# Optimization experiments

Measured on AMD Instinct MI355X. Metric: run time of the kernel, lower is better.

Reference implementation:

```python
import jax, jax.numpy as jnp
import numpy as np

N_NODES = 50000
N_EDGES = 1600000
IN_DIM = 1024
HID = 128
N_GRAPHS = 64


def setup_inputs() -> dict:
    key = jax.random.key(0)
    ks = jax.random.split(key, 8)
    x = jax.random.normal(ks[0], (N_NODES, IN_DIM), dtype=jnp.float32)
    edge_index = jax.random.randint(ks[1], (2, N_EDGES), 0, N_NODES, dtype=jnp.int32)
    batch = jnp.sort(jax.random.randint(ks[2], (N_NODES,), 0, N_GRAPHS, dtype=jnp.int32))
    # GATConv parameters (single head, concat irrelevant for 1 head)
    glorot = 1.0 / np.sqrt(IN_DIM)
    W = jax.random.uniform(ks[3], (IN_DIM, HID), minval=-glorot, maxval=glorot, dtype=jnp.float32)
    ga = 1.0 / np.sqrt(HID)
    att_src = jax.random.uniform(ks[4], (HID,), minval=-ga, maxval=ga, dtype=jnp.float32)
    att_dst = jax.random.uniform(ks[5], (HID,), minval=-ga, maxval=ga, dtype=jnp.float32)
    bias = jnp.zeros((HID,), dtype=jnp.float32)
    return {"x": x, "W": W, "att_src": att_src, "att_dst": att_dst, "bias": bias,
            "edge_index": edge_index, "batch": batch, "num_graphs": N_GRAPHS}


def reference(x, W, att_src, att_dst, bias, edge_index, batch, num_graphs):
    N = x.shape[0]
    h = x @ W                               # [N, HID]
    # add self-loops (GATConv default add_self_loops=True)
    loops = jnp.arange(N, dtype=edge_index.dtype)
    src = jnp.concatenate([edge_index[0], loops])   # [E+N]
    dst = jnp.concatenate([edge_index[1], loops])
    a_src = h @ att_src                     # [N]
    a_dst = h @ att_dst                     # [N]
    e = jax.nn.leaky_relu(a_src[src] + a_dst[dst], negative_slope=0.2)  # [E+N]
    # scatter-softmax over incoming edges of each destination node
    m = jax.ops.segment_max(e, dst, num_segments=N)
    p = jnp.exp(e - m[dst])
    denom = jax.ops.segment_sum(p, dst, num_segments=N)
    alpha = p / denom[dst]                  # [E+N]
    # attention-weighted aggregation
    out = jax.ops.segment_sum(alpha[:, None] * h[src], dst, num_segments=N)  # [N, HID]
    out = jax.nn.relu(out + bias)
    # global max pool over graphs in the batch
    return jax.ops.segment_max(out, batch, num_segments=num_graphs)          # [G, HID]
```

## Files before the change

### kernel.cpp

```cpp
#include <hip/hip_runtime.h>
#include <hip/hip_bf16.h>

#define N_NODES 50000
#define N_EDGES 1600000
#define IN_DIM 1024
#define HID 128
#define AGG_WAVES 6144

typedef __bf16 bf16x8 __attribute__((ext_vector_type(8)));
typedef float f32x4 __attribute__((ext_vector_type(4)));
typedef __bf16 bf16x4 __attribute__((ext_vector_type(4)));

__device__ __forceinline__ float2 bf2f(unsigned u) {
    return make_float2(__uint_as_float(u << 16), __uint_as_float(u & 0xffff0000u));
}
__device__ __forceinline__ float lrelu(float v) { return v > 0.f ? v : 0.2f * v; }
__device__ __forceinline__ float f16tof(unsigned bits) {
    return (float)__builtin_bit_cast(_Float16, (unsigned short)bits);
}

__global__ void prep_kernel(const float* __restrict__ W, __bf16* __restrict__ wt,
                            int* __restrict__ deg, float* __restrict__ out, int out_n) {
    int i = blockIdx.x * 256 + threadIdx.x;
    if (i < N_NODES) deg[i] = 0;
    if (i < out_n) out[i] = 0.0f;
    if (i < HID * IN_DIM) {
        int n = i >> 10, k = i & 1023;
        wt[i] = (__bf16)W[(size_t)k * HID + n];
    }
}

__global__ __launch_bounds__(256) void gemm_kernel(const float* __restrict__ x,
                                                   const __bf16* __restrict__ wt,
                                                   __bf16* __restrict__ h2,
                                                   const float* __restrict__ att_s,
                                                   const float* __restrict__ att_d,
                                                   float* __restrict__ o_as,
                                                   float* __restrict__ o_ad,
                                                   float* __restrict__ o_ps) {
    __shared__ __bf16 xa[2][64][40];
    __shared__ __bf16 wb[2][128][40];
    const int t = threadIdx.x;
    const int m0 = blockIdx.x * 64;
    const int wid = t >> 6, lane = t & 63;
    const int lm = lane & 15, q8 = (lane >> 4) * 8;
    const int rw0 = wid * 16;

    float4 xs_reg[2];
    uint2  ws_reg[4];

    auto stage_regs = [&](int k0) {
#pragma unroll
        for (int l = 0; l < 2; ++l) {
            int f = t + l * 256;
            int row = f >> 3, kq = f & 7;
            int gr = m0 + row;
            float4 v = make_float4(0.f, 0.f, 0.f, 0.f);
            if (gr < N_NODES)
                v = *(const float4*)(x + (size_t)gr * IN_DIM + k0 + kq * 4);
            xs_reg[l] = v;
        }
#pragma unroll
        for (int l = 0; l < 4; ++l) {
            int f = t + l * 256;
            int n = f >> 3, c = f & 7;
            ws_reg[l] = *(const uint2*)(wt + (size_t)n * IN_DIM + k0 + c * 4);
        }
    };
    auto regs_to_lds = [&](int b) {
#pragma unroll
        for (int l = 0; l < 2; ++l) {
            int f = t + l * 256;
            int row = f >> 3, kq = f & 7;
            bf16x4 v;
            v[0] = (__bf16)xs_reg[l].x; v[1] = (__bf16)xs_reg[l].y;
            v[2] = (__bf16)xs_reg[l].z; v[3] = (__bf16)xs_reg[l].w;
            *(bf16x4*)&xa[b][row][kq * 4] = v;
        }
#pragma unroll
        for (int l = 0; l < 4; ++l) {
            int f = t + l * 256;
            int n = f >> 3, c = f & 7;
            *(uint2*)&wb[b][n][c * 4] = ws_reg[l];
        }
    };

    f32x4 acc[8] = {};
    stage_regs(0);
    regs_to_lds(0);
    __syncthreads();
    for (int it = 0; it < 32; ++it) {
        const int cur = it & 1;
        if (it + 1 < 32) stage_regs((it + 1) * 32);
        bf16x8 af = *(const bf16x8*)&xa[cur][rw0 + lm][q8];
#pragma unroll
        for (int ct = 0; ct < 8; ++ct) {
            bf16x8 bfr = *(const bf16x8*)&wb[cur][ct * 16 + lm][q8];
            acc[ct] = __builtin_amdgcn_mfma_f32_16x16x32_bf16(af, bfr, acc[ct], 0, 0, 0);
        }
        if (it + 1 < 32) {
            regs_to_lds(cur ^ 1);
            __syncthreads();
        }
    }
    const int quad = lane >> 4;
    float attsf[8], attdf[8];
#pragma unroll
    for (int ct = 0; ct < 8; ++ct) {
        attsf[ct] = att_s[ct * 16 + lm];
        attdf[ct] = att_d[ct * 16 + lm];
    }
#pragma unroll
    for (int reg = 0; reg < 4; ++reg) {
        int row = m0 + rw0 + quad * 4 + reg;
        float ps = 0.f, pd = 0.f;
#pragma unroll
        for (int ct = 0; ct < 8; ++ct) {
            float v = acc[ct][reg];
            ps = fmaf(v, attsf[ct], ps);
            pd = fmaf(v, attdf[ct], pd);
        }
#pragma unroll
        for (int o = 8; o; o >>= 1) {
            ps += __shfl_xor(ps, o);
            pd += __shfl_xor(pd, o);
        }
        if (row < N_NODES) {
            if (lm == 0) {
                o_as[row] = ps; o_ad[row] = pd;
                o_ps[row] = __expf(lrelu(ps + pd));
            }
#pragma unroll
            for (int ct = 0; ct < 8; ++ct)
                h2[(size_t)row * HID + ct * 16 + lm] = (__bf16)acc[ct][reg];
        }
    }
}

__global__ void hist_kernel(const int* __restrict__ ei, int* __restrict__ deg) {
    int e = blockIdx.x * 256 + threadIdx.x;
    if (e < N_EDGES) atomicAdd(&deg[ei[N_EDGES + e]], 1);
}

__global__ void scan1_kernel(const int* __restrict__ deg, int* __restrict__ bsum) {
    int b = blockIdx.x, t = threadIdx.x;
    int base = b * 1024 + t * 4;
    int s = 0;
#pragma unroll
    for (int j = 0; j < 4; ++j) {
        int idx = base + j;
        if (idx < N_NODES) s += deg[idx];
    }
    for (int o = 32; o; o >>= 1) s += __shfl_xor(s, o);
    __shared__ int wsum[4];
    int lane = t & 63, w = t >> 6;
    if (lane == 0) wsum[w] = s;
    __syncthreads();
    if (t == 0) bsum[b] = wsum[0] + wsum[1] + wsum[2] + wsum[3];
}

__global__ void scan2_kernel(const int* __restrict__ bsum, int* __restrict__ boff,
                             int* __restrict__ rowstart, int nb) {
    if (threadIdx.x == 0 && blockIdx.x == 0) {
        int run = 0;
        for (int i = 0; i < nb; ++i) { boff[i] = run; run += bsum[i]; }
        rowstart[N_NODES] = run;
    }
}

__global__ void scan3_kernel(const int* __restrict__ deg, const int* __restrict__ boff,
                             int* __restrict__ rowstart, int* __restrict__ cursor) {
    int b = blockIdx.x, t = threadIdx.x;
    int base = b * 1024 + t * 4;
    int v[4]; int s = 0;
#pragma unroll
    for (int j = 0; j < 4; ++j) {
        int idx = base + j;
        v[j] = (idx < N_NODES) ? deg[idx] : 0;
        s += v[j];
    }
    int lane = t & 63, w = t >> 6;
    int inc = s;
    for (int o = 1; o < 64; o <<= 1) {
        int u = __shfl_up(inc, o);
        if (lane >= o) inc += u;
    }
    __shared__ int wt[4];
    if (lane == 63) wt[w] = inc;
    __syncthreads();
    int woff = 0;
    for (int i = 0; i < w; ++i) woff += wt[i];
    int run = woff + inc - s + boff[b];
#pragma unroll
    for (int j = 0; j < 4; ++j) {
        int idx = base + j;
        if (idx < N_NODES) {
            rowstart[idx] = run;
            cursor[idx] = run;
            run += v[j];
        }
    }
}

__global__ void scatter_kernel(const int* __restrict__ ei, int* __restrict__ cursor,
                               unsigned* __restrict__ csrp, const float* __restrict__ a_src,
                               const float* __restrict__ a_dst) {
    int e = blockIdx.x * 256 + threadIdx.x;
    if (e >= N_EDGES) return;
    int s = ei[e], d = ei[N_EDGES + e];
    int slot = atomicAdd(&cursor[d], 1);
    float pe = __expf(lrelu(a_src[s] + a_dst[d]));
    unsigned short hb = __builtin_bit_cast(unsigned short, (_Float16)pe);
    csrp[slot] = (unsigned)s | ((unsigned)hb << 16);
}

__global__ __launch_bounds__(256, 6) void aggregate_kernel(
    const unsigned* __restrict__ h2u, const float* __restrict__ pself_a,
    const int* __restrict__ rowstart, const unsigned* __restrict__ csrp,
    const float* __restrict__ bias, const int* __restrict__ batch,
    float* __restrict__ out) {
    const int wid = threadIdx.x >> 6, lane = threadIdx.x & 63;
    const int w = blockIdx.x * 4 + wid;
    const int q = N_NODES / AGG_WAVES;
    const int r = N_NODES - q * AGG_WAVES;
    int n0 = w * q + (w < r ? w : r);
    int n1 = n0 + q + (w < r ? 1 : 0);
    const float b0 = bias[2 * lane], b1 = bias[2 * lane + 1];

    int gcur = -1;
    float m0 = 0.f, m1 = 0.f;
    for (int n = n0; n < n1; ++n) {
        int rs = rowstart[n], re = rowstart[n + 1];
        float psf = pself_a[n];
        float2 hv = bf2f(h2u[((unsigned)n << 6) | (unsigned)lane]);
        float denom = psf;
        float2 acc = make_float2(psf * hv.x, psf * hv.y);
        for (int base = rs; base < re; base += 64) {
            int cnt = re - base; if (cnt > 64) cnt = 64;
            unsigned sp = 0u;
            if (base + lane < re) sp = csrp[base + lane];
            for (int e = 0; e < cnt; e += 16) {
                unsigned bb[16], uu[16];
#pragma unroll
                for (int i = 0; i < 16; ++i) {
                    bb[i] = (unsigned)__shfl((int)sp, e + i);
                    uu[i] = h2u[((bb[i] & 0xffffu) << 6) | (unsigned)lane];
                }
#pragma unroll
                for (int i = 0; i < 16; ++i) {
                    float2 g = bf2f(uu[i]);
                    float p = f16tof(bb[i] >> 16);
                    acc.x = fmaf(p, g.x, acc.x);
                    acc.y = fmaf(p, g.y, acc.y);
                    denom += p;
                }
            }
        }
        float inv = 1.0f / denom;
        float o0 = fmaxf(fmaf(acc.x, inv, b0), 0.0f);
        float o1 = fmaxf(fmaf(acc.y, inv, b1), 0.0f);
        int g = batch[n];
        if (g != gcur) {
            if (gcur >= 0) {
                unsigned* outp = (unsigned*)(out + (size_t)gcur * HID);
                atomicMax(&outp[2 * lane], __float_as_uint(m0));
                atomicMax(&outp[2 * lane + 1], __float_as_uint(m1));
            }
            gcur = g; m0 = o0; m1 = o1;
        } else {
            m0 = fmaxf(m0, o0); m1 = fmaxf(m1, o1);
        }
    }
    if (gcur >= 0) {
        unsigned* outp = (unsigned*)(out + (size_t)gcur * HID);
        atomicMax(&outp[2 * lane], __float_as_uint(m0));
        atomicMax(&outp[2 * lane + 1], __float_as_uint(m1));
    }
}

extern "C" void kernel_launch(void* const* d_in, const int* in_sizes, int n_in,
                              void* d_out, int out_size, void* d_ws, size_t ws_size,
                              hipStream_t stream) {
    const float* x     = (const float*)d_in[0];
    const float* W     = (const float*)d_in[1];
    const float* att_s = (const float*)d_in[2];
    const float* att_d = (const float*)d_in[3];
    const float* bias  = (const float*)d_in[4];
    const int*   ei    = (const int*)d_in[5];
    const int*   batch = (const int*)d_in[6];
    float*       out   = (float*)d_out;

    char* ws = (char*)d_ws;
    size_t off = 0;
    auto alloc = [&](size_t bytes) -> void* {
        void* p = ws + off;
        off += (bytes + 255) & ~(size_t)255;
        return p;
    };
    const int NB = (N_NODES + 1023) / 1024;
    __bf16*   h2       = (__bf16*)alloc((size_t)N_NODES * HID * 2);
    __bf16*   wt       = (__bf16*)alloc((size_t)HID * IN_DIM * 2);
    float*    a_src    = (float*)alloc((size_t)N_NODES * 4);
    float*    a_dst    = (float*)alloc((size_t)N_NODES * 4);
    float*    pself    = (float*)alloc((size_t)N_NODES * 4);
    int*      deg      = (int*)alloc((size_t)N_NODES * 4);
    int*      rowstart = (int*)alloc((size_t)(N_NODES + 1) * 4);
    int*      cursor   = (int*)alloc((size_t)N_NODES * 4);
    int*      bsum     = (int*)alloc((size_t)NB * 4);
    int*      boff     = (int*)alloc((size_t)NB * 4);
    unsigned* csrp     = (unsigned*)alloc((size_t)N_EDGES * 4);
    (void)ws_size; (void)in_sizes; (void)n_in;

    hipLaunchKernelGGL(prep_kernel, dim3(512), dim3(256), 0, stream,
                       W, wt, deg, out, out_size);
    hipLaunchKernelGGL(gemm_kernel, dim3((N_NODES + 63) / 64), dim3(256), 0, stream,
                       x, wt, h2, att_s, att_d, a_src, a_dst, pself);
    hipLaunchKernelGGL(hist_kernel, dim3((N_EDGES + 255) / 256), dim3(256), 0, stream,
                       ei, deg);
    hipLaunchKernelGGL(scan1_kernel, dim3(NB), dim3(256), 0, stream, deg, bsum);
    hipLaunchKernelGGL(scan2_kernel, dim3(1), dim3(64), 0, stream, bsum, boff, rowstart, NB);
    hipLaunchKernelGGL(scan3_kernel, dim3(NB), dim3(256), 0, stream, deg, boff, rowstart, cursor);
    hipLaunchKernelGGL(scatter_kernel, dim3((N_EDGES + 255) / 256), dim3(256), 0, stream,
                       ei, cursor, csrp, a_src, a_dst);
    hipLaunchKernelGGL(aggregate_kernel, dim3(AGG_WAVES / 4), dim3(256), 0, stream,
                       (const unsigned*)h2, pself, rowstart, csrp, bias, batch, out);
}
```

Baseline: 524.0 us.

## Drop LDS staging in GEMM; load operands directly into registers per wave

The projection GEMM no longer stages x and W tiles through shared memory with block-wide barriers. Each wave loads its own 16 rows of x and the W fragments directly from global memory into registers, double-buffered across k-steps. This removes LDS traffic and synchronization, at the cost of redundant per-wave W loads through cache and higher register use.

```diff
diff --git a/kernel.cpp b/kernel.cpp
--- a/kernel.cpp
+++ b/kernel.cpp
@@ -38,69 +38,59 @@
                                                    float* __restrict__ o_as,
                                                    float* __restrict__ o_ad,
                                                    float* __restrict__ o_ps) {
-    __shared__ __bf16 xa[2][64][40];
-    __shared__ __bf16 wb[2][128][40];
     const int t = threadIdx.x;
-    const int m0 = blockIdx.x * 64;
     const int wid = t >> 6, lane = t & 63;
     const int lm = lane & 15, q8 = (lane >> 4) * 8;
-    const int rw0 = wid * 16;
-
-    float4 xs_reg[2];
-    uint2  ws_reg[4];
-
-    auto stage_regs = [&](int k0) {
-#pragma unroll
-        for (int l = 0; l < 2; ++l) {
-            int f = t + l * 256;
-            int row = f >> 3, kq = f & 7;
-            int gr = m0 + row;
-            float4 v = make_float4(0.f, 0.f, 0.f, 0.f);
-            if (gr < N_NODES)
-                v = *(const float4*)(x + (size_t)gr * IN_DIM + k0 + kq * 4);
-            xs_reg[l] = v;
-        }
-#pragma unroll
-        for (int l = 0; l < 4; ++l) {
-            int f = t + l * 256;
-            int n = f >> 3, c = f & 7;
-            ws_reg[l] = *(const uint2*)(wt + (size_t)n * IN_DIM + k0 + c * 4);
+    const int row0 = (blockIdx.x * 4 + wid) * 16;
+    const int gr = row0 + lm;
+    const bool arow_ok = (gr < N_NODES);
+    const float* __restrict__ xrow = x + (size_t)gr * IN_DIM + q8;
+    const __bf16* __restrict__ wrow = wt + (size_t)lm * IN_DIM + q8;
+
+    auto load_a = [&](int k0, float4& A0, float4& A1) {
+        if (arow_ok) {
+            A0 = *(const float4*)(xrow + k0);
+            A1 = *(const float4*)(xrow + k0 + 4);
+        } else {
+            A0 = make_float4(0.f, 0.f, 0.f, 0.f);
+            A1 = A0;
         }
     };
-    auto regs_to_lds = [&](int b) {
-#pragma unroll
-        for (int l = 0; l < 2; ++l) {
-            int f = t + l * 256;
-            int row = f >> 3, kq = f & 7;
-            bf16x4 v;
-            v[0] = (__bf16)xs_reg[l].x; v[1] = (__bf16)xs_reg[l].y;
-            v[2] = (__bf16)xs_reg[l].z; v[3] = (__bf16)xs_reg[l].w;
-            *(bf16x4*)&xa[b][row][kq * 4] = v;
-        }
-#pragma unroll
-        for (int l = 0; l < 4; ++l) {
-            int f = t + l * 256;
-            int n = f >> 3, c = f & 7;
-            *(uint2*)&wb[b][n][c * 4] = ws_reg[l];
-        }
+    auto load_b = [&](int k0, uint4* B) {
+#pragma unroll
+        for (int ct = 0; ct < 8; ++ct)
+            B[ct] = *(const uint4*)(wrow + (size_t)ct * 16 * IN_DIM + k0);
     };
+    auto cvt_a = [&](const float4& A0, const float4& A1) {
+        bf16x8 af;
+        af[0] = (__bf16)A0.x; af[1] = (__bf16)A0.y;
+        af[2] = (__bf16)A0.z; af[3] = (__bf16)A0.w;
+        af[4] = (__bf16)A1.x; af[5] = (__bf16)A1.y;
+        af[6] = (__bf16)A1.z; af[7] = (__bf16)A1.w;
+        return af;
+    };
 
     f32x4 acc[8] = {};
-    stage_regs(0);
-    regs_to_lds(0);
-    __syncthreads();
-    for (int it = 0; it < 32; ++it) {
-        const int cur = it & 1;
-        if (it + 1 < 32) stage_regs((it + 1) * 32);
-        bf16x8 af = *(const bf16x8*)&xa[cur][rw0 + lm][q8];
-#pragma unroll
-        for (int ct = 0; ct < 8; ++ct) {
-            bf16x8 bfr = *(const bf16x8*)&wb[cur][ct * 16 + lm][q8];
-            acc[ct] = __builtin_amdgcn_mfma_f32_16x16x32_bf16(af, bfr, acc[ct], 0, 0, 0);
-        }
+    float4 A0a, A1a, A0b, A1b;
+    uint4 Ba[8], Bb[8];
+    load_a(0, A0a, A1a);
+    load_b(0, Ba);
+    for (int it = 0; it < 32; it += 2) {
+        if (it + 1 < 32) { load_a((it + 1) * 32, A0b, A1b); load_b((it + 1) * 32, Bb); }
+        {
+            bf16x8 af = cvt_a(A0a, A1a);
+#pragma unroll
+            for (int ct = 0; ct < 8; ++ct)
+                acc[ct] = __builtin_amdgcn_mfma_f32_16x16x32_bf16(
+                    af, *(const bf16x8*)&Ba[ct], acc[ct], 0, 0, 0);
+        }
+        if (it + 2 < 32) { load_a((it + 2) * 32, A0a, A1a); load_b((it + 2) * 32, Ba); }
         if (it + 1 < 32) {
-            regs_to_lds(cur ^ 1);
-            __syncthreads();
+            bf16x8 af = cvt_a(A0b, A1b);
+#pragma unroll
+            for (int ct = 0; ct < 8; ++ct)
+                acc[ct] = __builtin_amdgcn_mfma_f32_16x16x32_bf16(
+                    af, *(const bf16x8*)&Bb[ct], acc[ct], 0, 0, 0);
         }
     }
     const int quad = lane >> 4;
@@ -112,7 +102,7 @@
     }
 #pragma unroll
     for (int reg = 0; reg < 4; ++reg) {
-        int row = m0 + rw0 + quad * 4 + reg;
+        int row = row0 + quad * 4 + reg;
         float ps = 0.f, pd = 0.f;
 #pragma unroll
         for (int ct = 0; ct < 8; ++ct) {
```

After: 652.7 us. +24.6%, slower.

## Stage GEMM epilogue through LDS and reuse histogram atomic slots for CSR scatter

Applied to the files above, without the earlier changes.

The GEMM epilogue now writes the bf16 h tile into shared memory, aliased with the operand buffers through a union, and then each thread writes contiguous 64-byte row chunks. This replaces the scattered 2-byte stores. The histogram kernel keeps the return value of its atomicAdd as a per-edge position, so the scatter kernel computes its slot as rowstart plus that position and drops its second pass of atomics on a cursor array. The cost is an extra 6.4MB epos buffer that is written and then read, plus two more block barriers in the GEMM.

```diff
diff --git a/kernel.cpp b/kernel.cpp
--- a/kernel.cpp
+++ b/kernel.cpp
@@ -38,8 +38,10 @@
                                                    float* __restrict__ o_as,
                                                    float* __restrict__ o_ad,
                                                    float* __restrict__ o_ps) {
-    __shared__ __bf16 xa[2][64][40];
-    __shared__ __bf16 wb[2][128][40];
+    __shared__ union {
+        struct { __bf16 xa[2][64][40]; __bf16 wb[2][128][40]; } s;
+        __bf16 ep[64][132];
+    } u;
     const int t = threadIdx.x;
     const int m0 = blockIdx.x * 64;
     const int wid = t >> 6, lane = t & 63;
@@ -75,13 +77,13 @@
             bf16x4 v;
             v[0] = (__bf16)xs_reg[l].x; v[1] = (__bf16)xs_reg[l].y;
             v[2] = (__bf16)xs_reg[l].z; v[3] = (__bf16)xs_reg[l].w;
-            *(bf16x4*)&xa[b][row][kq * 4] = v;
+            *(bf16x4*)&u.s.xa[b][row][kq * 4] = v;
         }
 #pragma unroll
         for (int l = 0; l < 4; ++l) {
             int f = t + l * 256;
             int n = f >> 3, c = f & 7;
-            *(uint2*)&wb[b][n][c * 4] = ws_reg[l];
+            *(uint2*)&u.s.wb[b][n][c * 4] = ws_reg[l];
         }
     };
 
@@ -92,10 +94,10 @@
     for (int it = 0; it < 32; ++it) {
         const int cur = it & 1;
         if (it + 1 < 32) stage_regs((it + 1) * 32);
-        bf16x8 af = *(const bf16x8*)&xa[cur][rw0 + lm][q8];
+        bf16x8 af = *(const bf16x8*)&u.s.xa[cur][rw0 + lm][q8];
 #pragma unroll
         for (int ct = 0; ct < 8; ++ct) {
-            bf16x8 bfr = *(const bf16x8*)&wb[cur][ct * 16 + lm][q8];
+            bf16x8 bfr = *(const bf16x8*)&u.s.wb[cur][ct * 16 + lm][q8];
             acc[ct] = __builtin_amdgcn_mfma_f32_16x16x32_bf16(af, bfr, acc[ct], 0, 0, 0);
         }
         if (it + 1 < 32) {
@@ -125,21 +127,37 @@
             ps += __shfl_xor(ps, o);
             pd += __shfl_xor(pd, o);
         }
-        if (row < N_NODES) {
-            if (lm == 0) {
-                o_as[row] = ps; o_ad[row] = pd;
-                o_ps[row] = __expf(lrelu(ps + pd));
-            }
-#pragma unroll
-            for (int ct = 0; ct < 8; ++ct)
-                h2[(size_t)row * HID + ct * 16 + lm] = (__bf16)acc[ct][reg];
-        }
-    }
-}
-
-__global__ void hist_kernel(const int* __restrict__ ei, int* __restrict__ deg) {
+        if (row < N_NODES && lm == 0) {
+            o_as[row] = ps; o_ad[row] = pd;
+            o_ps[row] = __expf(lrelu(ps + pd));
+        }
+    }
+    __syncthreads();
+#pragma unroll
+    for (int reg = 0; reg < 4; ++reg) {
+        int lrow = rw0 + quad * 4 + reg;
+#pragma unroll
+        for (int ct = 0; ct < 8; ++ct)
+            u.ep[lrow][ct * 16 + lm] = (__bf16)acc[ct][reg];
+    }
+    __syncthreads();
+    {
+        int lr = t >> 2, qt = t & 3;
+        int grow = m0 + lr;
+        if (grow < N_NODES) {
+            uint2* dst = (uint2*)(h2 + (size_t)grow * HID + qt * 32);
+            const __bf16* srcp = &u.ep[lr][qt * 32];
+#pragma unroll
+            for (int j = 0; j < 8; ++j)
+                dst[j] = *(const uint2*)(srcp + j * 4);
+        }
+    }
+}
+
+__global__ void hist_kernel(const int* __restrict__ ei, int* __restrict__ deg,
+                            int* __restrict__ epos) {
     int e = blockIdx.x * 256 + threadIdx.x;
-    if (e < N_EDGES) atomicAdd(&deg[ei[N_EDGES + e]], 1);
+    if (e < N_EDGES) epos[e] = atomicAdd(&deg[ei[N_EDGES + e]], 1);
 }
 
 __global__ void scan1_kernel(const int* __restrict__ deg, int* __restrict__ bsum) {
@@ -169,7 +187,7 @@
 }
 
 __global__ void scan3_kernel(const int* __restrict__ deg, const int* __restrict__ boff,
-                             int* __restrict__ rowstart, int* __restrict__ cursor) {
+                             int* __restrict__ rowstart) {
     int b = blockIdx.x, t = threadIdx.x;
     int base = b * 1024 + t * 4;
     int v[4]; int s = 0;
@@ -196,22 +214,20 @@
         int idx = base + j;
         if (idx < N_NODES) {
             rowstart[idx] = run;
-            cursor[idx] = run;
             run += v[j];
         }
     }
 }
 
-__global__ void scatter_kernel(const int* __restrict__ ei, int* __restrict__ cursor,
-                               unsigned* __restrict__ csrp, const float* __restrict__ a_src,
-                               const float* __restrict__ a_dst) {
+__global__ void scatter_kernel(const int* __restrict__ ei, const int* __restrict__ rowstart,
+                               const int* __restrict__ epos, unsigned* __restrict__ csrp,
+                               const float* __restrict__ a_src, const float* __restrict__ a_dst) {
     int e = blockIdx.x * 256 + threadIdx.x;
     if (e >= N_EDGES) return;
     int s = ei[e], d = ei[N_EDGES + e];
-    int slot = atomicAdd(&cursor[d], 1);
     float pe = __expf(lrelu(a_src[s] + a_dst[d]));
     unsigned short hb = __builtin_bit_cast(unsigned short, (_Float16)pe);
-    csrp[slot] = (unsigned)s | ((unsigned)hb << 16);
+    csrp[rowstart[d] + epos[e]] = (unsigned)s | ((unsigned)hb << 16);
 }
 
 __global__ __launch_bounds__(256, 6) void aggregate_kernel(
@@ -305,9 +321,9 @@
     float*    pself    = (float*)alloc((size_t)N_NODES * 4);
     int*      deg      = (int*)alloc((size_t)N_NODES * 4);
     int*      rowstart = (int*)alloc((size_t)(N_NODES + 1) * 4);
-    int*      cursor   = (int*)alloc((size_t)N_NODES * 4);
     int*      bsum     = (int*)alloc((size_t)NB * 4);
     int*      boff     = (int*)alloc((size_t)NB * 4);
+    int*      epos     = (int*)alloc((size_t)N_EDGES * 4);
     unsigned* csrp     = (unsigned*)alloc((size_t)N_EDGES * 4);
     (void)ws_size; (void)in_sizes; (void)n_in;
 
@@ -316,12 +332,12 @@
     hipLaunchKernelGGL(gemm_kernel, dim3((N_NODES + 63) / 64), dim3(256), 0, stream,
                        x, wt, h2, att_s, att_d, a_src, a_dst, pself);
     hipLaunchKernelGGL(hist_kernel, dim3((N_EDGES + 255) / 256), dim3(256), 0, stream,
-                       ei, deg);
+                       ei, deg, epos);
     hipLaunchKernelGGL(scan1_kernel, dim3(NB), dim3(256), 0, stream, deg, bsum);
     hipLaunchKernelGGL(scan2_kernel, dim3(1), dim3(64), 0, stream, bsum, boff, rowstart, NB);
-    hipLaunchKernelGGL(scan3_kernel, dim3(NB), dim3(256), 0, stream, deg, boff, rowstart, cursor);
+    hipLaunchKernelGGL(scan3_kernel, dim3(NB), dim3(256), 0, stream, deg, boff, rowstart);
     hipLaunchKernelGGL(scatter_kernel, dim3((N_EDGES + 255) / 256), dim3(256), 0, stream,
-                       ei, cursor, csrp, a_src, a_dst);
+                       ei, rowstart, epos, csrp, a_src, a_dst);
     hipLaunchKernelGGL(aggregate_kernel, dim3(AGG_WAVES / 4), dim3(256), 0, stream,
                        (const unsigned*)h2, pself, rowstart, csrp, bias, batch, out);
 }
```

Measured after the change: 503.3 us. 4.0% less time.
